# Performance work log

Measured on AMD Instinct MI355X. Metric: run time of the kernel, lower is better.

The kernel has to match this reference:

```python
import jax, jax.numpy as jnp
import numpy as np

B, H, W, C = 8, 256, 256, 180
HEADS, HEAD_DIM = 6, 30
WIN = (16, 16)
SPARSITY = 4


def setup_inputs() -> dict:
    key = jax.random.key(0)
    ks = jax.random.split(key, 6)
    bg = 1.0 / np.sqrt(3 * HEAD_DIM)          # ExpertGather init bound (1/sqrt(head_dim_out)) approx
    bs = 1.0 / np.sqrt(C * HEADS)             # ExpertScatter init bound
    return {
        "x": jax.random.normal(ks[0], (B, H, W, C), jnp.float32),
        "Wr": jax.random.normal(ks[1], (HEADS, C), jnp.float32) / np.sqrt(C),      # router Linear(dim, heads, bias=False)
        "Wqkv": jax.random.uniform(ks[2], (HEADS, C, 3 * HEAD_DIM), jnp.float32, -bg, bg),
        "Wo": jax.random.uniform(ks[3], (HEADS, HEAD_DIM, C), jnp.float32, -bs, bs),
        "Wp": jax.random.normal(ks[4], (C, C), jnp.float32) / np.sqrt(C),          # proj Linear(dim, dim)
        "bp": jnp.zeros((C,), jnp.float32),
    }


def reference(x, Wr, Wqkv, Wo, Wp, bp):
    wh, ww = WIN
    L = wh * ww  # tokens per window = 256
    # ---- window_partition: (B,H,W,C) -> (Bw, L, C)
    xw = x.reshape(B, H // wh, wh, W // ww, ww, C).transpose(0, 1, 3, 2, 4, 5).reshape(-1, L, C)
    Bw = xw.shape[0]
    # ---- router: sigmoid(Linear) -> (Bw, L, heads)
    logits = jax.nn.sigmoid(jnp.einsum('blc,ec->ble', xw, Wr))
    k = min(max(L // SPARSITY, 2), L)  # static: 64
    # ---- top-k including first token (get_topk_includefirst)
    tail = logits[:, 1:, :].transpose(0, 2, 1)          # (Bw, heads, L-1)
    tv, ti = jax.lax.top_k(tail, k - 1)                 # top k-1 over tokens 1..L-1
    ti = ti + 1
    fv = logits[:, 0, :][:, :, None]                    # (Bw, heads, 1)
    fi = jnp.zeros((Bw, HEADS, 1), jnp.int32)
    vals = jnp.concatenate([fv, tv], axis=2)            # (Bw, heads, k) sigmoid gates
    idx = jnp.concatenate([fi, ti], axis=2)             # (Bw, heads, k) token indices
    idx_flat = idx.reshape(Bw, HEADS * k)
    # ---- ExpertGather: per-head gather then per-head linear -> QKV
    Xg = jnp.take_along_axis(xw, idx_flat[:, :, None], axis=1).reshape(Bw, HEADS, k, C)
    qkv = jnp.einsum('beki,eij->bekj', Xg, Wqkv)        # (Bw, heads, k, 3*head_dim)
    Q, K, V = jnp.split(qkv, 3, axis=-1)
    # ---- scaled dot product attention over the k routed tokens per head
    scores = jnp.einsum('bekd,bejd->bekj', Q, K) / np.sqrt(HEAD_DIM).astype(np.float32)
    attn = jnp.einsum('bekj,bejd->bekd', jax.nn.softmax(scores, axis=-1), V)
    attn = attn * vals[..., None]                       # sigmoid gating
    # ---- ExpertScatter: per-head linear then scatter-add combine
    pre = jnp.einsum('bekj,eji->beki', attn, Wo)        # (Bw, heads, k, C)
    scattered = jnp.zeros((Bw, L, C), x.dtype).at[
        jnp.arange(Bw)[:, None], idx_flat
    ].add(pre.reshape(Bw, HEADS * k, C))
    # ---- window_reverse: (Bw, L, C) -> (B, H, W, C)
    y = scattered.reshape(B, H // wh, W // ww, wh, ww, C).transpose(0, 1, 3, 2, 4, 5).reshape(B, H, W, C)
    # ---- output projection (dropout prob = 0)
    return jnp.einsum('bhwc,oc->bhwo', y, Wp) + bp
```

## Files before the change

### kernel.cpp

```cpp
#include <hip/hip_runtime.h>
#include <math.h>

#define NB 8
#define NH 256
#define NW 256
#define NC 180
#define NE 6
#define HD 30
#define NL 256
#define NK 64
#define NWIN 2048

typedef __attribute__((ext_vector_type(8))) short bf16x8;
typedef __attribute__((ext_vector_type(4))) float f32x4;

union FU { bf16x8 f; unsigned u[4]; unsigned short s[8]; };

static __device__ __forceinline__ unsigned short f2bf(float x) {
    unsigned u = __float_as_uint(x);
    unsigned r = (u + 0x7FFFu + ((u >> 16) & 1u)) >> 16;
    return (unsigned short)r;
}
static __device__ __forceinline__ unsigned pk2(float a, float b) {
    return (unsigned)f2bf(a) | ((unsigned)f2bf(b) << 16);
}
static __device__ __forceinline__ bf16x8 ld8(const unsigned short* p) {
    FU t;
    *(uint2*)&t.u[0] = *(const uint2*)p;
    *(uint2*)&t.u[2] = *(const uint2*)(p + 16);
    return t.f;
}
static __device__ __forceinline__ bf16x8 ld8q(const unsigned short* p) {
    FU t;
    t.u[0] = *(const unsigned*)p;
    t.u[1] = *(const unsigned*)(p + 2);
    t.u[2] = *(const unsigned*)(p + 16);
    t.u[3] = *(const unsigned*)(p + 18);
    return t.f;
}
static __device__ __forceinline__ bf16x8 pack8(float4 a, float4 b) {
    FU t;
    t.u[0] = pk2(a.x, a.y); t.u[1] = pk2(a.z, a.w);
    t.u[2] = pk2(b.x, b.y); t.u[3] = pk2(b.z, b.w);
    return t.f;
}

__global__ __launch_bounds__(256) void k_prep(
    const float* __restrict__ Wqkv, const float* __restrict__ Wo,
    const float* __restrict__ Wp,
    unsigned short* __restrict__ Wqkv_t, unsigned short* __restrict__ Wcomb_t)
{
    int i = blockIdx.x * 256 + threadIdx.x;
    if (i < NE * 96 * 192) {
        int h = i / (96 * 192), rm = i % (96 * 192), np = rm / 192, k = rm % 192;
        int sec = np >> 5, r = np & 31;
        float v = (r < 30 && k < NC) ? Wqkv[((long)h * NC + k) * 90 + sec * 30 + r] : 0.f;
        Wqkv_t[i] = f2bf(v);
    }
    if (i < NE * 192 * 32) {
        int h = i / (192 * 32), rm = i % (192 * 32), o = rm / 32, d = rm & 31;
        float acc = 0.f;
        if (o < NC && d < HD) {
            const float* wo = Wo + ((long)h * HD + d) * NC;
            const float* wp = Wp + (long)o * NC;
            for (int c = 0; c < NC; ++c) acc += wo[c] * wp[c];
        }
        Wcomb_t[i] = f2bf(acc);
    }
}

__global__ __launch_bounds__(256) void k_router_topk(
    const float* __restrict__ x, const float* __restrict__ Wr,
    int* __restrict__ idx_g, float* __restrict__ vals_g)
{
    __shared__ float wr_s[NE * NC];
    __shared__ __align__(16) float xs[32 * 181];
    __shared__ float lg[NE * NL];

    const int w   = blockIdx.x;
    const int tid = threadIdx.x;
    const int b = w >> 8, hb = (w >> 4) & 15, wb = w & 15;
    const long win_base = (((long)b * NH + hb * 16) * NW + wb * 16) * NC;

    for (int f = tid; f < NE * NC; f += 256) wr_s[f] = Wr[f];
    __syncthreads();

    for (int tile = 0; tile < 8; ++tile) {
        for (int f = tid; f < 32 * NC; f += 256) {
            int tl = f / NC, ch = f % NC;
            int tok = tile * 32 + tl;
            int r = tok >> 4, cl = tok & 15;
            xs[tl * 181 + ch] = x[win_base + ((long)r * NW + cl) * NC + ch];
        }
        __syncthreads();
        if (tid < 192) {
            int tl = tid & 31, e = tid >> 5;
            float acc = 0.f;
            for (int c = 0; c < NC; ++c) acc += xs[tl * 181 + c] * wr_s[e * NC + c];
            lg[e * NL + tile * 32 + tl] = 1.0f / (1.0f + expf(-acc));
        }
        __syncthreads();
    }

    unsigned long long* keys = (unsigned long long*)xs;
    #pragma unroll
    for (int e = 0; e < NE; ++e) {
        unsigned kb = __float_as_uint(lg[e * NL + tid]);
        unsigned long long comp =
            ((unsigned long long)kb << 32) | (unsigned)(0xFFFFFFFFu - tid);
        if (tid == 0) comp = 0ull;
        keys[e * NL + tid] = comp;
    }
    __syncthreads();

    for (int k = 2; k <= 256; k <<= 1) {
        for (int j = k >> 1; j > 0; j >>= 1) {
            const int i = tid, ixj = i ^ j;
            if (ixj > i) {
                const bool up = ((i & k) == 0);
                #pragma unroll
                for (int e = 0; e < NE; ++e) {
                    unsigned long long a  = keys[e * NL + i];
                    unsigned long long bv = keys[e * NL + ixj];
                    bool sw = up ? (a < bv) : (a > bv);
                    if (sw) { keys[e * NL + i] = bv; keys[e * NL + ixj] = a; }
                }
            }
            __syncthreads();
        }
    }

    if (tid < NK - 1) {
        #pragma unroll
        for (int e = 0; e < NE; ++e) {
            unsigned long long kk = keys[e * NL + tid];
            int t = (int)(0xFFFFFFFFu - (unsigned)kk);
            idx_g[(w * NE + e) * NK + 1 + tid]  = t;
            vals_g[(w * NE + e) * NK + 1 + tid] = __uint_as_float((unsigned)(kk >> 32));
        }
    }
    if (tid == 0) {
        #pragma unroll
        for (int e = 0; e < NE; ++e) {
            idx_g[(w * NE + e) * NK]  = 0;
            vals_g[(w * NE + e) * NK] = lg[e * NL];
        }
    }
}

__global__ __launch_bounds__(256, 3) void k_attn(
    const float* __restrict__ x,
    const unsigned short* __restrict__ Wqkv_t,
    const int* __restrict__ idx_g, const float* __restrict__ vals_g,
    unsigned short* __restrict__ at_g)
{
    __shared__ char sm[34816];
    const int tid = threadIdx.x;
    const int wv = tid >> 6;
    const int ln = tid & 63;
    const int lr = ln & 15;
    const int lg = ln >> 4;

    const int id = blockIdx.x * 4 + wv;
    const int w = id / 6;
    const int h = id % 6;
    const int b = w >> 8, hb = (w >> 4) & 15, wb = w & 15;
    const long win_base = (((long)b * NH + hb * 16) * NW + wb * 16) * NC;

    unsigned short* q_s = (unsigned short*)(sm + wv * 8704);
    unsigned short* k_s = q_s + 2176;

    int tokr[4];
    #pragma unroll
    for (int t = 0; t < 4; ++t)
        tokr[t] = idx_g[((long)w * NE + h) * NK + 16 * t + lr];

    f32x4 acc[6][4];
    #pragma unroll
    for (int nt = 0; nt < 6; ++nt)
        #pragma unroll
        for (int mt = 0; mt < 4; ++mt) acc[nt][mt] = (f32x4){0.f, 0.f, 0.f, 0.f};

    const unsigned short* bb = Wqkv_t + ((long)h * 96 + lr) * 192 + 4 * lg;
    #pragma unroll
    for (int kt = 0; kt < 6; ++kt) {
        bf16x8 Amt[4];
        #pragma unroll
        for (int mt = 0; mt < 4; ++mt) {
            const float* xr = x + win_base +
                ((long)(tokr[mt] >> 4) * NW + (tokr[mt] & 15)) * NC;
            if (kt < 5) {
                float4 a  = *(const float4*)(xr + 4 * lg + 32 * kt);
                float4 b2 = *(const float4*)(xr + 4 * lg + 32 * kt + 16);
                Amt[mt] = pack8(a, b2);
            } else {
                float4 a  = *(const float4*)(xr + 4 * lg + 160);
                float4 b2 = make_float4(0.f, 0.f, 0.f, 0.f);
                if (lg == 0) b2 = *(const float4*)(xr + 176);
                Amt[mt] = pack8(a, b2);
            }
        }
        #pragma unroll
        for (int nt = 0; nt < 6; ++nt) {
            bf16x8 B = ld8(bb + nt * (16 * 192) + kt * 32);
            #pragma unroll
            for (int mt = 0; mt < 4; ++mt)
                acc[nt][mt] = __builtin_amdgcn_mfma_f32_16x16x32_bf16(Amt[mt], B, acc[nt][mt], 0, 0, 0);
        }
    }

    #pragma unroll
    for (int nt = 0; nt < 4; ++nt) {
        unsigned short* dst = (nt < 2 ? q_s : k_s) + 16 * (nt & 1) + lr;
        #pragma unroll
        for (int mt = 0; mt < 4; ++mt) {
            int row = 16 * mt + 4 * lg;
            dst[(row + 0) * 34] = f2bf(acc[nt][mt][0]);
            dst[(row + 1) * 34] = f2bf(acc[nt][mt][1]);
            dst[(row + 2) * 34] = f2bf(acc[nt][mt][2]);
            dst[(row + 3) * 34] = f2bf(acc[nt][mt][3]);
        }
    }
    unsigned V32[4][2][2];
    #pragma unroll
    for (int j = 0; j < 2; ++j)
        #pragma unroll
        for (int mt = 0; mt < 4; ++mt) {
            V32[mt][j][0] = pk2(acc[4 + j][mt][0], acc[4 + j][mt][1]);
            V32[mt][j][1] = pk2(acc[4 + j][mt][2], acc[4 + j][mt][3]);
        }

    __syncthreads();

    f32x4 s[4][4];
    {
        bf16x8 Bq[4];
        #pragma unroll
        for (int nt = 0; nt < 4; ++nt)
            Bq[nt] = ld8q(q_s + (16 * nt + lr) * 34 + 4 * lg);
        #pragma unroll
        for (int amt = 0; amt < 4; ++amt) {
            bf16x8 Ak = ld8q(k_s + (16 * amt + lr) * 34 + 4 * lg);
            #pragma unroll
            for (int nt = 0; nt < 4; ++nt)
                s[amt][nt] = __builtin_amdgcn_mfma_f32_16x16x32_bf16(
                    Ak, Bq[nt], (f32x4){0.f, 0.f, 0.f, 0.f}, 0, 0, 0);
        }
    }

    float gsc[4];
    #pragma unroll
    for (int nt = 0; nt < 4; ++nt) {
        float mx = -1e30f;
        #pragma unroll
        for (int amt = 0; amt < 4; ++amt)
            #pragma unroll
            for (int r = 0; r < 4; ++r) mx = fmaxf(mx, s[amt][nt][r]);
        mx = fmaxf(mx, __shfl_xor(mx, 16));
        mx = fmaxf(mx, __shfl_xor(mx, 32));
        float sum = 0.f;
        #pragma unroll
        for (int amt = 0; amt < 4; ++amt)
            #pragma unroll
            for (int r = 0; r < 4; ++r) {
                float p = __expf((s[amt][nt][r] - mx) * 0.18257418583505536f);
                s[amt][nt][r] = p;
                sum += p;
            }
        sum += __shfl_xor(sum, 16);
        sum += __shfl_xor(sum, 32);
        gsc[nt] = vals_g[((long)w * NE + h) * NK + 16 * nt + lr] / sum;
    }

    bf16x8 Av[2][2];
    #pragma unroll
    for (int amt = 0; amt < 2; ++amt)
        #pragma unroll
        for (int kt = 0; kt < 2; ++kt) {
            FU t;
            t.u[0] = V32[2 * kt][amt][0];
            t.u[1] = V32[2 * kt][amt][1];
            t.u[2] = V32[2 * kt + 1][amt][0];
            t.u[3] = V32[2 * kt + 1][amt][1];
            Av[amt][kt] = t.f;
        }
    #pragma unroll
    for (int nt = 0; nt < 4; ++nt) {
        bf16x8 Pb[2];
        float g = gsc[nt];
        #pragma unroll
        for (int kt = 0; kt < 2; ++kt) {
            FU t;
            t.u[0] = pk2(s[2 * kt][nt][0] * g, s[2 * kt][nt][1] * g);
            t.u[1] = pk2(s[2 * kt][nt][2] * g, s[2 * kt][nt][3] * g);
            t.u[2] = pk2(s[2 * kt + 1][nt][0] * g, s[2 * kt + 1][nt][1] * g);
            t.u[3] = pk2(s[2 * kt + 1][nt][2] * g, s[2 * kt + 1][nt][3] * g);
            Pb[kt] = t.f;
        }
        f32x4 a0 = (f32x4){0.f, 0.f, 0.f, 0.f};
        a0 = __builtin_amdgcn_mfma_f32_16x16x32_bf16(Av[0][0], Pb[0], a0, 0, 0, 0);
        a0 = __builtin_amdgcn_mfma_f32_16x16x32_bf16(Av[0][1], Pb[1], a0, 0, 0, 0);
        f32x4 a1 = (f32x4){0.f, 0.f, 0.f, 0.f};
        a1 = __builtin_amdgcn_mfma_f32_16x16x32_bf16(Av[1][0], Pb[0], a1, 0, 0, 0);
        a1 = __builtin_amdgcn_mfma_f32_16x16x32_bf16(Av[1][1], Pb[1], a1, 0, 0, 0);
        unsigned short* row = at_g + (((long)h * NWIN + w) * 64 + 16 * nt + lr) * 32;
        *(uint2*)(row + 4 * lg)      = make_uint2(pk2(a0[0], a0[1]), pk2(a0[2], a0[3]));
        *(uint2*)(row + 16 + 4 * lg) = make_uint2(pk2(a1[0], a1[1]), pk2(a1[2], a1[3]));
    }
}

__global__ __launch_bounds__(384) void k_scatter(
    const unsigned short* __restrict__ at_g,
    const unsigned short* __restrict__ Wcomb_t,
    const float* __restrict__ bp,
    const int* __restrict__ idx_g,
    float* __restrict__ out)
{
    __shared__ float outf[256 * 49];
    __shared__ unsigned char idx_s[NE * NK];

    const int p = blockIdx.x;
    const int w = blockIdx.y;
    const int tid = threadIdx.x;
    const int b = w >> 8, hb = (w >> 4) & 15, wb = w & 15;

    const int wv = tid >> 6;
    const int ln = tid & 63;
    const int lr = ln & 15;
    const int lg = ln >> 4;

    if (tid < NE * NK) idx_s[tid] = (unsigned char)idx_g[(long)w * NE * NK + tid];
    for (int f = tid; f < 256 * 49; f += 384) outf[f] = 0.f;
    __syncthreads();

    const int wcol = wv % 3;
    const int nth  = wv / 3;
    #pragma unroll 1
    for (int h = 0; h < NE; ++h) {
        bf16x8 Aw = ld8(Wcomb_t + ((long)h * 192 + p * 48 + 16 * wcol + lr) * 32 + 4 * lg);
        #pragma unroll
        for (int t = 0; t < 2; ++t) {
            const int nt = 2 * nth + t;
            bf16x8 Bt = ld8(at_g + (((long)h * NWIN + w) * 64 + 16 * nt + lr) * 32 + 4 * lg);
            f32x4 acc = __builtin_amdgcn_mfma_f32_16x16x32_bf16(
                Aw, Bt, (f32x4){0.f, 0.f, 0.f, 0.f}, 0, 0, 0);
            int tok = idx_s[h * NK + 16 * nt + lr];
            float* dst = outf + tok * 49 + 16 * wcol + 4 * lg;
            dst[0] += acc[0];
            dst[1] += acc[1];
            dst[2] += acc[2];
            dst[3] += acc[3];
        }
        __syncthreads();
    }

    const int cl2 = (p == 3) ? 18 : 24;
    for (int f = tid; f < 256 * cl2; f += 384) {
        int t = f / cl2, j = f % cl2;
        int c = 48 * p + 2 * j;
        float2 o;
        o.x = outf[t * 49 + 2 * j]     + bp[c];
        o.y = outf[t * 49 + 2 * j + 1] + bp[c + 1];
        long obase = (((long)b * NH + hb * 16 + (t >> 4)) * NW + wb * 16 + (t & 15)) * NC + c;
        *(float2*)(out + obase) = o;
    }
}

extern "C" void kernel_launch(void* const* d_in, const int* in_sizes, int n_in,
                              void* d_out, int out_size, void* d_ws, size_t ws_size,
                              hipStream_t stream) {
    const float* x    = (const float*)d_in[0];
    const float* Wr   = (const float*)d_in[1];
    const float* Wqkv = (const float*)d_in[2];
    const float* Wo   = (const float*)d_in[3];
    const float* Wp   = (const float*)d_in[4];
    const float* bp   = (const float*)d_in[5];
    float* out = (float*)d_out;

    char* ws = (char*)d_ws;
    unsigned short* Wqkv_t  = (unsigned short*)ws;
    unsigned short* Wcomb_t = (unsigned short*)(ws + 221184);
    int*   idx_g  = (int*)(ws + 294912);
    float* vals_g = (float*)(ws + 294912 + (size_t)NWIN * NE * NK * 4);
    unsigned short* at_g = (unsigned short*)(ws + 294912 + 2 * (size_t)NWIN * NE * NK * 4);

    k_prep<<<432, 256, 0, stream>>>(Wqkv, Wo, Wp, Wqkv_t, Wcomb_t);
    k_router_topk<<<NWIN, 256, 0, stream>>>(x, Wr, idx_g, vals_g);
    k_attn<<<3072, 256, 0, stream>>>(x, Wqkv_t, idx_g, vals_g, at_g);
    k_scatter<<<dim3(4, NWIN), 384, 0, stream>>>(at_g, Wcomb_t, bp, idx_g, out);
}
```

Baseline: 650.4 us.

## Pre-convert x to bf16 and fold scatter column tiles into one block

Adds a kernel that converts the whole input x to bf16 in the workspace, so the attention gather reads half the bytes and skips per-load packing. The scatter kernel now runs one block per window that loops over the four output column tiles. It loads the attention outputs and token indices once into registers instead of once per column-tile block. The cost is an extra full pass over x (read fp32, write bf16) and less block-level parallelism in the scatter.

```diff
diff --git a/kernel.cpp b/kernel.cpp
--- a/kernel.cpp
+++ b/kernel.cpp
@@ -38,11 +38,19 @@
     t.u[3] = *(const unsigned*)(p + 18);
     return t.f;
 }
-static __device__ __forceinline__ bf16x8 pack8(float4 a, float4 b) {
-    FU t;
-    t.u[0] = pk2(a.x, a.y); t.u[1] = pk2(a.z, a.w);
-    t.u[2] = pk2(b.x, b.y); t.u[3] = pk2(b.z, b.w);
-    return t.f;
+
+__global__ __launch_bounds__(256) void k_xbf(
+    const float* __restrict__ x, unsigned short* __restrict__ xbf)
+{
+    long i = ((long)blockIdx.x * 256 + threadIdx.x) * 8;
+    float4 a = *(const float4*)(x + i);
+    float4 b = *(const float4*)(x + i + 4);
+    uint4 o;
+    o.x = pk2(a.x, a.y);
+    o.y = pk2(a.z, a.w);
+    o.z = pk2(b.x, b.y);
+    o.w = pk2(b.z, b.w);
+    *(uint4*)(xbf + i) = o;
 }
 
 __global__ __launch_bounds__(256) void k_prep(
@@ -149,7 +157,7 @@
 }
 
 __global__ __launch_bounds__(256, 3) void k_attn(
-    const float* __restrict__ x,
+    const unsigned short* __restrict__ xbf,
     const unsigned short* __restrict__ Wqkv_t,
     const int* __restrict__ idx_g, const float* __restrict__ vals_g,
     unsigned short* __restrict__ at_g)
@@ -187,17 +195,16 @@
         bf16x8 Amt[4];
         #pragma unroll
         for (int mt = 0; mt < 4; ++mt) {
-            const float* xr = x + win_base +
+            const unsigned short* xr = xbf + win_base +
                 ((long)(tokr[mt] >> 4) * NW + (tokr[mt] & 15)) * NC;
             if (kt < 5) {
-                float4 a  = *(const float4*)(xr + 4 * lg + 32 * kt);
-                float4 b2 = *(const float4*)(xr + 4 * lg + 32 * kt + 16);
-                Amt[mt] = pack8(a, b2);
+                Amt[mt] = ld8(xr + 4 * lg + 32 * kt);
             } else {
-                float4 a  = *(const float4*)(xr + 4 * lg + 160);
-                float4 b2 = make_float4(0.f, 0.f, 0.f, 0.f);
-                if (lg == 0) b2 = *(const float4*)(xr + 176);
-                Amt[mt] = pack8(a, b2);
+                FU t;
+                *(uint2*)&t.u[0] = *(const uint2*)(xr + 160 + 4 * lg);
+                *(uint2*)&t.u[2] = (lg == 0) ? *(const uint2*)(xr + 176)
+                                             : make_uint2(0u, 0u);
+                Amt[mt] = t.f;
             }
         }
         #pragma unroll
@@ -319,8 +326,7 @@
     __shared__ float outf[256 * 49];
     __shared__ unsigned char idx_s[NE * NK];
 
-    const int p = blockIdx.x;
-    const int w = blockIdx.y;
+    const int w = blockIdx.x;
     const int tid = threadIdx.x;
     const int b = w >> 8, hb = (w >> 4) & 15, wb = w & 15;
 
@@ -329,40 +335,60 @@
     const int lr = ln & 15;
     const int lg = ln >> 4;
 
-    if (tid < NE * NK) idx_s[tid] = (unsigned char)idx_g[(long)w * NE * NK + tid];
-    for (int f = tid; f < 256 * 49; f += 384) outf[f] = 0.f;
-    __syncthreads();
+    idx_s[tid] = (unsigned char)idx_g[(long)w * NE * NK + tid];
 
     const int wcol = wv % 3;
     const int nth  = wv / 3;
-    #pragma unroll 1
-    for (int h = 0; h < NE; ++h) {
-        bf16x8 Aw = ld8(Wcomb_t + ((long)h * 192 + p * 48 + 16 * wcol + lr) * 32 + 4 * lg);
+
+    bf16x8 Bt[NE][2];
+    #pragma unroll
+    for (int h = 0; h < NE; ++h)
         #pragma unroll
         for (int t = 0; t < 2; ++t) {
             const int nt = 2 * nth + t;
-            bf16x8 Bt = ld8(at_g + (((long)h * NWIN + w) * 64 + 16 * nt + lr) * 32 + 4 * lg);
-            f32x4 acc = __builtin_amdgcn_mfma_f32_16x16x32_bf16(
-                Aw, Bt, (f32x4){0.f, 0.f, 0.f, 0.f}, 0, 0, 0);
-            int tok = idx_s[h * NK + 16 * nt + lr];
-            float* dst = outf + tok * 49 + 16 * wcol + 4 * lg;
-            dst[0] += acc[0];
-            dst[1] += acc[1];
-            dst[2] += acc[2];
-            dst[3] += acc[3];
-        }
+            Bt[h][t] = ld8(at_g + (((long)h * NWIN + w) * 64 + 16 * nt + lr) * 32 + 4 * lg);
+        }
+    __syncthreads();
+
+    int tokk[NE][2];
+    #pragma unroll
+    for (int h = 0; h < NE; ++h)
+        #pragma unroll
+        for (int t = 0; t < 2; ++t)
+            tokk[h][t] = idx_s[h * NK + 16 * (2 * nth + t) + lr];
+
+    #pragma unroll 1
+    for (int p = 0; p < 4; ++p) {
+        for (int f = tid; f < 256 * 49; f += 384) outf[f] = 0.f;
         __syncthreads();
-    }
-
-    const int cl2 = (p == 3) ? 18 : 24;
-    for (int f = tid; f < 256 * cl2; f += 384) {
-        int t = f / cl2, j = f % cl2;
-        int c = 48 * p + 2 * j;
-        float2 o;
-        o.x = outf[t * 49 + 2 * j]     + bp[c];
-        o.y = outf[t * 49 + 2 * j + 1] + bp[c + 1];
-        long obase = (((long)b * NH + hb * 16 + (t >> 4)) * NW + wb * 16 + (t & 15)) * NC + c;
-        *(float2*)(out + obase) = o;
+
+        #pragma unroll 1
+        for (int h = 0; h < NE; ++h) {
+            bf16x8 Aw = ld8(Wcomb_t + ((long)h * 192 + p * 48 + 16 * wcol + lr) * 32 + 4 * lg);
+            #pragma unroll
+            for (int t = 0; t < 2; ++t) {
+                f32x4 acc = __builtin_amdgcn_mfma_f32_16x16x32_bf16(
+                    Aw, Bt[h][t], (f32x4){0.f, 0.f, 0.f, 0.f}, 0, 0, 0);
+                float* dst = outf + tokk[h][t] * 49 + 16 * wcol + 4 * lg;
+                dst[0] += acc[0];
+                dst[1] += acc[1];
+                dst[2] += acc[2];
+                dst[3] += acc[3];
+            }
+            __syncthreads();
+        }
+
+        const int cl2 = (p == 3) ? 18 : 24;
+        for (int f = tid; f < 256 * cl2; f += 384) {
+            int t = f / cl2, j = f % cl2;
+            int c = 48 * p + 2 * j;
+            float2 o;
+            o.x = outf[t * 49 + 2 * j]     + bp[c];
+            o.y = outf[t * 49 + 2 * j + 1] + bp[c + 1];
+            long obase = (((long)b * NH + hb * 16 + (t >> 4)) * NW + wb * 16 + (t & 15)) * NC + c;
+            *(float2*)(out + obase) = o;
+        }
+        __syncthreads();
     }
 }
 
@@ -383,9 +409,11 @@
     int*   idx_g  = (int*)(ws + 294912);
     float* vals_g = (float*)(ws + 294912 + (size_t)NWIN * NE * NK * 4);
     unsigned short* at_g = (unsigned short*)(ws + 294912 + 2 * (size_t)NWIN * NE * NK * 4);
+    unsigned short* xbf  = at_g + (size_t)NE * NWIN * 64 * 32;
 
     k_prep<<<432, 256, 0, stream>>>(Wqkv, Wo, Wp, Wqkv_t, Wcomb_t);
+    k_xbf<<<46080, 256, 0, stream>>>(x, xbf);
     k_router_topk<<<NWIN, 256, 0, stream>>>(x, Wr, idx_g, vals_g);
-    k_attn<<<3072, 256, 0, stream>>>(x, Wqkv_t, idx_g, vals_g, at_g);
-    k_scatter<<<dim3(4, NWIN), 384, 0, stream>>>(at_g, Wcomb_t, bp, idx_g, out);
-}
+    k_attn<<<3072, 256, 0, stream>>>(xbf, Wqkv_t, idx_g, vals_g, at_g);
+    k_scatter<<<NWIN, 384, 0, stream>>>(at_g, Wcomb_t, bp, idx_g, out);
+}
```

Result: slower. 768.0 us (+18.1%).

## Merge scatter column-chunk blocks into one block per window with register-held attention tiles

Applied to the files above, without the earlier changes.

The scatter kernel now launches one block per window instead of four (one per 48-column chunk). Each block loads the attention output tiles and token indices once into registers, then loops over the four column chunks, reusing them from registers. This removes three redundant reloads of at_g and idx per window. The store path is widened from float2 to float4, and launch bounds now request two blocks per CU. In exchange there are fewer blocks, each doing serial work with extra syncs, and register pressure is higher.

```diff
diff --git a/kernel.cpp b/kernel.cpp
--- a/kernel.cpp
+++ b/kernel.cpp
@@ -309,7 +309,7 @@
     }
 }
 
-__global__ __launch_bounds__(384) void k_scatter(
+__global__ __launch_bounds__(384, 2) void k_scatter(
     const unsigned short* __restrict__ at_g,
     const unsigned short* __restrict__ Wcomb_t,
     const float* __restrict__ bp,
@@ -319,8 +319,7 @@
     __shared__ float outf[256 * 49];
     __shared__ unsigned char idx_s[NE * NK];
 
-    const int p = blockIdx.x;
-    const int w = blockIdx.y;
+    const int w = blockIdx.x;
     const int tid = threadIdx.x;
     const int b = w >> 8, hb = (w >> 4) & 15, wb = w & 15;
 
@@ -329,40 +328,62 @@
     const int lr = ln & 15;
     const int lg = ln >> 4;
 
-    if (tid < NE * NK) idx_s[tid] = (unsigned char)idx_g[(long)w * NE * NK + tid];
-    for (int f = tid; f < 256 * 49; f += 384) outf[f] = 0.f;
-    __syncthreads();
+    idx_s[tid] = (unsigned char)idx_g[(long)w * NE * NK + tid];
 
     const int wcol = wv % 3;
     const int nth  = wv / 3;
-    #pragma unroll 1
-    for (int h = 0; h < NE; ++h) {
-        bf16x8 Aw = ld8(Wcomb_t + ((long)h * 192 + p * 48 + 16 * wcol + lr) * 32 + 4 * lg);
+
+    bf16x8 Bt[NE][2];
+    #pragma unroll
+    for (int h = 0; h < NE; ++h)
         #pragma unroll
         for (int t = 0; t < 2; ++t) {
             const int nt = 2 * nth + t;
-            bf16x8 Bt = ld8(at_g + (((long)h * NWIN + w) * 64 + 16 * nt + lr) * 32 + 4 * lg);
-            f32x4 acc = __builtin_amdgcn_mfma_f32_16x16x32_bf16(
-                Aw, Bt, (f32x4){0.f, 0.f, 0.f, 0.f}, 0, 0, 0);
-            int tok = idx_s[h * NK + 16 * nt + lr];
-            float* dst = outf + tok * 49 + 16 * wcol + 4 * lg;
-            dst[0] += acc[0];
-            dst[1] += acc[1];
-            dst[2] += acc[2];
-            dst[3] += acc[3];
-        }
+            Bt[h][t] = ld8(at_g + (((long)h * NWIN + w) * 64 + 16 * nt + lr) * 32 + 4 * lg);
+        }
+    __syncthreads();
+
+    int tokk[NE][2];
+    #pragma unroll
+    for (int h = 0; h < NE; ++h)
+        #pragma unroll
+        for (int t = 0; t < 2; ++t)
+            tokk[h][t] = idx_s[h * NK + 16 * (2 * nth + t) + lr];
+
+    #pragma unroll 1
+    for (int p = 0; p < 4; ++p) {
+        for (int f = tid; f < 256 * 49; f += 384) outf[f] = 0.f;
         __syncthreads();
-    }
-
-    const int cl2 = (p == 3) ? 18 : 24;
-    for (int f = tid; f < 256 * cl2; f += 384) {
-        int t = f / cl2, j = f % cl2;
-        int c = 48 * p + 2 * j;
-        float2 o;
-        o.x = outf[t * 49 + 2 * j]     + bp[c];
-        o.y = outf[t * 49 + 2 * j + 1] + bp[c + 1];
-        long obase = (((long)b * NH + hb * 16 + (t >> 4)) * NW + wb * 16 + (t & 15)) * NC + c;
-        *(float2*)(out + obase) = o;
+
+        #pragma unroll 1
+        for (int h = 0; h < NE; ++h) {
+            bf16x8 Aw = ld8(Wcomb_t + ((long)h * 192 + p * 48 + 16 * wcol + lr) * 32 + 4 * lg);
+            #pragma unroll
+            for (int t = 0; t < 2; ++t) {
+                f32x4 acc = __builtin_amdgcn_mfma_f32_16x16x32_bf16(
+                    Aw, Bt[h][t], (f32x4){0.f, 0.f, 0.f, 0.f}, 0, 0, 0);
+                float* dst = outf + tokk[h][t] * 49 + 16 * wcol + 4 * lg;
+                dst[0] += acc[0];
+                dst[1] += acc[1];
+                dst[2] += acc[2];
+                dst[3] += acc[3];
+            }
+            __syncthreads();
+        }
+
+        const int nf4 = (p == 3) ? 9 : 12;
+        for (int f = tid; f < 256 * nf4; f += 384) {
+            int t = f / nf4, j = f % nf4;
+            int c = 48 * p + 4 * j;
+            float4 o;
+            o.x = outf[t * 49 + 4 * j]     + bp[c];
+            o.y = outf[t * 49 + 4 * j + 1] + bp[c + 1];
+            o.z = outf[t * 49 + 4 * j + 2] + bp[c + 2];
+            o.w = outf[t * 49 + 4 * j + 3] + bp[c + 3];
+            long obase = (((long)b * NH + hb * 16 + (t >> 4)) * NW + wb * 16 + (t & 15)) * NC + c;
+            *(float4*)(out + obase) = o;
+        }
+        __syncthreads();
     }
 }
 
@@ -387,5 +408,5 @@
     k_prep<<<432, 256, 0, stream>>>(Wqkv, Wo, Wp, Wqkv_t, Wcomb_t);
     k_router_topk<<<NWIN, 256, 0, stream>>>(x, Wr, idx_g, vals_g);
     k_attn<<<3072, 256, 0, stream>>>(x, Wqkv_t, idx_g, vals_g, at_g);
-    k_scatter<<<dim3(4, NWIN), 384, 0, stream>>>(at_g, Wcomb_t, bp, idx_g, out);
-}
+    k_scatter<<<NWIN, 384, 0, stream>>>(at_g, Wcomb_t, bp, idx_g, out);
+}
```

Result: slower. 687.4 us (+5.7%).
